# Kernel tuning notes

Measured on AMD Instinct MI355X. Metric: run time of the kernel, lower is better.

The kernel has to match this reference:

```python
import jax, jax.numpy as jnp
import numpy as np
from jax import lax

N_ITER = 50  # entmax-bisect iterations (entmax library default)
DEG = 12    # neighbors per node in global item graph


def entmax_bisect(X, alpha):
    # entmax with per-row alpha, over axis=1. X: [B, L, 1], alpha: [B, 1, 1]
    d = X.shape[1]
    Xa = X * (alpha - 1.0)
    inv = 1.0 / (alpha - 1.0)
    _p = lambda z: jnp.maximum(z, 0.0) ** inv
    max_val = jnp.max(Xa, axis=1, keepdims=True)
    tau_lo = max_val - 1.0                                   # _gp(1, alpha) = 1
    tau_hi = max_val - jnp.power(1.0 / d, alpha - 1.0)       # _gp(1/d, alpha)
    f_lo = jnp.sum(_p(Xa - tau_lo), axis=1, keepdims=True) - 1.0

    def body(i, carry):
        tau_lo, dm, _ = carry
        dm = dm * 0.5
        tau_m = tau_lo + dm
        f_m = jnp.sum(_p(Xa - tau_m), axis=1, keepdims=True) - 1.0
        tau_lo = jnp.where(f_m * f_lo >= 0.0, tau_m, tau_lo)
        return (tau_lo, dm, tau_m)

    tau_lo, dm, tau_m = lax.fori_loop(0, N_ITER, body, (tau_lo, tau_hi - tau_lo, tau_lo))
    p_m = _p(Xa - tau_m)
    return p_m / jnp.sum(p_m, axis=1, keepdims=True)  # ensure_sum_one


def setup_inputs() -> dict:
    key = jax.random.key(0)
    ks = jax.random.split(key, 10)
    B, L, D, N = 1024, 50, 256, 40000
    E = N * DEG
    stdv = 1.0 / np.sqrt(D)
    u = lambda k, shape: jax.random.uniform(k, shape, jnp.float32, -stdv, stdv)

    item_emb = u(ks[0], (N, D)).at[0].set(0.0)  # padding_idx=0
    items = jax.random.randint(ks[1], (B, L), 0, N)
    inputs_seq = jax.random.randint(ks[2], (B, L), 0, N)
    alias_inputs = jax.random.randint(ks[3], (B, L), 0, L)
    target_embedding = jax.random.normal(ks[4], (B, 1, 2 * D), jnp.float32)

    # sparse global item adjacency (row-normalized, DEG neighbors per node)
    adj_rows = jnp.repeat(jnp.arange(N, dtype=jnp.int32), DEG)
    adj_cols = jax.random.randint(ks[5], (E,), 0, N, dtype=jnp.int32)
    adj_vals = jax.random.uniform(ks[6], (E,), jnp.float32) / DEG

    kp = jax.random.split(ks[7], 10)
    return {
        "items": items, "inputs_seq": inputs_seq, "alias_inputs": alias_inputs,
        "target_embedding": target_embedding, "item_emb": item_emb,
        "adj_rows": adj_rows, "adj_cols": adj_cols, "adj_vals": adj_vals,
        "wf_w": u(kp[0], (D, 2 * D)), "wf_b": u(kp[1], (D,)),
        "alphaw_w": u(kp[2], (1, D)), "alphaw_b": u(kp[3], (1,)),
        "at_w0": u(kp[4], (1, D)), "at_w1": u(kp[5], (D, D)),
        "at_w2": u(kp[6], (D, D)), "at_bias": u(kp[7], (D,)),
    }


def reference(items, inputs_seq, alias_inputs, target_embedding, item_emb,
              adj_rows, adj_cols, adj_vals, wf_w, wf_b, alphaw_w, alphaw_b,
              at_w0, at_w1, at_w2, at_bias):
    N = item_emb.shape[0]
    # GlobalItemConv (1 layer): h = (x + adj @ x) / 2 via sparse SpMM
    agg = jax.ops.segment_sum(adj_vals[:, None] * item_emb[adj_cols], adj_rows,
                              num_segments=N)
    graph_embs = (item_emb + agg) * 0.5

    hidden = graph_embs[items]                              # [B, L, D] (dropout: eval)
    target_emb = target_embedding @ wf_w.T + wf_b           # [B, 1, D]

    # get_alpha: sigmoid + 1, then masked_fill(==1 -> 1.00001)
    alpha_ent = jax.nn.sigmoid(target_emb @ alphaw_w.T + alphaw_b) + 1.0  # [B,1,1]
    alpha_ent = jnp.where(alpha_ent == 1.0, 1.00001, alpha_ent)

    # tglobal_attention
    scores = jax.nn.relu(hidden @ at_w1 + target_emb @ at_w2 + at_bias) @ at_w0.T  # [B,L,1]
    attn = entmax_bisect(scores, alpha_ent)                 # sparse softmax over L
    c = jnp.einsum('blo,bld->bod', attn, hidden)[:, 0, :]   # alpha^T @ v, squeeze -> [B,D]

    c = jax.nn.selu(c)
    return c / jnp.linalg.norm(c, axis=-1, keepdims=True)
```

## Files before the change

### kernel.cpp

```cpp
#include <hip/hip_runtime.h>
#include <hip/hip_bf16.h>
#include <math.h>

#define BB 1024
#define LL 50
#define DD 256
#define TWO_D 512
#define NN 40000
#define DEG 12
#define NITER 50

typedef __attribute__((ext_vector_type(8))) short short8;
typedef __attribute__((ext_vector_type(4))) float floatx4;

__device__ __forceinline__ float wave_sum64(float v) {
#pragma unroll
    for (int off = 32; off > 0; off >>= 1) v += __shfl_xor(v, off, 64);
    return v;
}
__device__ __forceinline__ float wave_max64(float v) {
#pragma unroll
    for (int off = 32; off > 0; off >>= 1) v = fmaxf(v, __shfl_xor(v, off, 64));
    return v;
}
__device__ __forceinline__ float dpp_sum64(float v) {
#define DPPADD(ctrl, rm, bm) \
    v += __int_as_float(__builtin_amdgcn_update_dpp(0, __float_as_int(v), ctrl, rm, bm, true))
    DPPADD(0x111, 0xF, 0xF);
    DPPADD(0x112, 0xF, 0xF);
    DPPADD(0x114, 0xF, 0xE);
    DPPADD(0x118, 0xF, 0xC);
    DPPADD(0x142, 0xA, 0xF);
    DPPADD(0x143, 0xC, 0xF);
#undef DPPADD
    return __int_as_float(__builtin_amdgcn_readlane(__float_as_int(v), 63));
}
__device__ __forceinline__ float bf2f(ushort u) {
    union { unsigned int i; float f; } c; c.i = ((unsigned int)u) << 16; return c.f;
}
__device__ __forceinline__ ushort f2bf(float f) {
    __hip_bfloat16 h = __float2bfloat16(f);
    return *(ushort*)&h;
}
__device__ __forceinline__ float hw_exp2(float x) { return __builtin_amdgcn_exp2f(x); }
__device__ __forceinline__ float hw_log2(float x) { return __builtin_amdgcn_logf(x); }

__global__ __launch_bounds__(256) void k_stage1(
    const float* __restrict__ emb, ushort* __restrict__ ebf,
    const int* __restrict__ items, int* __restrict__ flags,
    const float* __restrict__ wf_w, const float* __restrict__ wf_b,
    const float* __restrict__ at_w2, const float* __restrict__ at_bias,
    const float* __restrict__ aw, const float* __restrict__ ab,
    const float* __restrict__ at_w1,
    float* __restrict__ Wc, float* __restrict__ v,
    float* __restrict__ bc, float* __restrict__ c0,
    ushort* __restrict__ w1t)
{
    __shared__ float wcol[DD];
    __shared__ float4 s_p[4][64];
    __shared__ float wred[4];
    __shared__ ushort s_t[4][DD];
    int bid = blockIdx.x;
    int tid = threadIdx.x;

    if (bid < 512) {
        int k = bid;
        int lane = tid & 63, wv = tid >> 6;
        int ng = tid & 63;
        int dq = tid >> 6;

        wcol[tid] = wf_w[tid * TWO_D + k];
        __syncthreads();

        float4 acc = {0.f, 0.f, 0.f, 0.f};
        const float4* w24 = (const float4*)at_w2;
#pragma unroll 8
        for (int d = dq * 64; d < dq * 64 + 64; ++d) {
            float4 w2 = w24[d * 64 + ng];
            float wc = wcol[d];
            acc.x += wc * w2.x; acc.y += wc * w2.y;
            acc.z += wc * w2.z; acc.w += wc * w2.w;
        }
        s_p[dq][ng] = acc;

        float s1 = wcol[tid] * aw[tid];
        s1 = wave_sum64(s1);
        if (lane == 0) wred[wv] = s1;
        __syncthreads();
        if (tid == 0) v[k] = wred[0] + wred[1] + wred[2] + wred[3];

        if (tid < 64) {
            float4 r0 = s_p[0][tid], r1 = s_p[1][tid];
            float4 r2 = s_p[2][tid], r3 = s_p[3][tid];
            float4 rr;
            rr.x = (r0.x + r1.x) + (r2.x + r3.x);
            rr.y = (r0.y + r1.y) + (r2.y + r3.y);
            rr.z = (r0.z + r1.z) + (r2.z + r3.z);
            rr.w = (r0.w + r1.w) + (r2.w + r3.w);
            *(float4*)(Wc + k * DD + tid * 4) = rr;
        }

        if (k < 64) {
            int k0 = k * 4;
#pragma unroll
            for (int j = 0; j < 4; ++j)
                s_t[j][tid] = f2bf(at_w1[(k0 + j) * DD + tid]);
            __syncthreads();
            ushort4 pk;
            pk.x = s_t[0][tid]; pk.y = s_t[1][tid];
            pk.z = s_t[2][tid]; pk.w = s_t[3][tid];
            *(ushort4*)(w1t + tid * DD + k0) = pk;
        }

        if (k == 0) {
            __syncthreads();
            wcol[tid] = wf_b[tid];
            __syncthreads();
            float b[8];
#pragma unroll
            for (int j = 0; j < 8; ++j) b[j] = 0.f;
#pragma unroll 4
            for (int d = 0; d < DD; d += 8) {
#pragma unroll
                for (int j = 0; j < 8; ++j)
                    b[j] += wcol[d + j] * at_w2[(d + j) * DD + tid];
            }
            bc[tid] = at_bias[tid] + ((b[0] + b[1]) + (b[2] + b[3]))
                                   + ((b[4] + b[5]) + (b[6] + b[7]));
            float s2 = wcol[tid] * aw[tid];
            s2 = wave_sum64(s2);
            if (lane == 0) wred[wv] = s2;
            __syncthreads();
            if (tid == 0) c0[0] = wred[0] + wred[1] + wred[2] + wred[3] + ab[0];
        }
    } else if (bid < 712) {
        int i = (bid - 512) * 256 + tid;
        flags[items[i]] = 1;
    } else {
        int base4 = (bid - 712) * (256 * 8) + tid;
        float4 val[8];
#pragma unroll
        for (int j = 0; j < 8; ++j)
            val[j] = *(const float4*)(emb + (size_t)(base4 + j * 256) * 4);
#pragma unroll
        for (int j = 0; j < 8; ++j) {
            ushort4 o;
            o.x = f2bf(val[j].x); o.y = f2bf(val[j].y);
            o.z = f2bf(val[j].z); o.w = f2bf(val[j].w);
            *(ushort4*)(ebf + (size_t)(base4 + j * 256) * 4) = o;
        }
    }
}

__global__ __launch_bounds__(256) void k_stage2(
    const ushort* __restrict__ ebf, const int* __restrict__ adj_cols,
    const float* __restrict__ adj_vals, const int* __restrict__ flags,
    ushort* __restrict__ gbf,
    const float* __restrict__ tgt, const float* __restrict__ Wc,
    const float* __restrict__ bc, const float* __restrict__ v,
    const float* __restrict__ c0, float* __restrict__ t2,
    float* __restrict__ alpha)
{
    __shared__ float x_s[4 * TWO_D];
    int bid = blockIdx.x;
    int tid = threadIdx.x;
    int wv = tid >> 6, lane = tid & 63;

    if (bid < 1024) {
        int t = bid;
        int btile = t >> 2, ntile = t & 3;
        int b0 = btile * 4, n0 = ntile * 64;
        int j = wv;
        for (int i = tid; i < 4 * TWO_D; i += 256) x_s[i] = tgt[b0 * TWO_D + i];
        __syncthreads();

        float acc = bc[n0 + lane];
        const float* xr = x_s + j * TWO_D;
#pragma unroll 8
        for (int k = 0; k < TWO_D; ++k)
            acc += xr[k] * Wc[k * DD + n0 + lane];
        t2[(b0 + j) * DD + n0 + lane] = acc;

        if (ntile == 0) {
            float s = 0.f;
#pragma unroll
            for (int i = 0; i < 8; ++i) s += xr[lane + 64 * i] * v[lane + 64 * i];
            s = wave_sum64(s);
            if (lane == 0) {
                float a = 1.f + 1.f / (1.f + expf(-(s + c0[0])));
                if (a == 1.f) a = 1.00001f;
                alpha[b0 + j] = a;
            }
        }
    } else {
        int n = (bid - 1024) * 4 + wv;
        if (flags[n] != 1) return;
        int colv = 0; float valv = 0.f;
        if (lane < DEG) { colv = adj_cols[n * DEG + lane]; valv = adj_vals[n * DEG + lane]; }
        int cols[DEG]; float vals[DEG];
#pragma unroll
        for (int k = 0; k < DEG; ++k) {
            cols[k] = __builtin_amdgcn_readlane(colv, k);
            vals[k] = __int_as_float(__builtin_amdgcn_readlane(__float_as_int(valv), k));
        }
        ushort4 s = *(const ushort4*)(ebf + (size_t)n * DD + lane * 4);
        ushort4 e[DEG];
#pragma unroll
        for (int k = 0; k < DEG; ++k)
            e[k] = *(const ushort4*)(ebf + (size_t)cols[k] * DD + lane * 4);
        float a0 = bf2f(s.x), a1 = bf2f(s.y), a2 = bf2f(s.z), a3 = bf2f(s.w);
#pragma unroll
        for (int k = 0; k < DEG; ++k) {
            float vv = vals[k];
            a0 += vv * bf2f(e[k].x); a1 += vv * bf2f(e[k].y);
            a2 += vv * bf2f(e[k].z); a3 += vv * bf2f(e[k].w);
        }
        ushort4 o;
        o.x = f2bf(0.5f * a0); o.y = f2bf(0.5f * a1);
        o.z = f2bf(0.5f * a2); o.w = f2bf(0.5f * a3);
        *(ushort4*)(gbf + (size_t)n * DD + lane * 4) = o;
    }
}

__device__ __forceinline__ float pw(float z, float invv) {
    return hw_exp2(invv * hw_log2(z));
}

__global__ __launch_bounds__(256, 4) void k_fused(
    const int* __restrict__ items, const ushort* __restrict__ gbf,
    const ushort* __restrict__ w1t, const float* __restrict__ t2,
    const float* __restrict__ at_w0, const float* __restrict__ alpha,
    float* __restrict__ out)
{
    __shared__ float t2_s[DD];
    __shared__ float sred[64][4];
    __shared__ int s_items[64];
    __shared__ float red[4];

    int b = blockIdx.x;
    int tid = threadIdx.x;
    int lane = tid & 63, wv = tid >> 6;
    int cn = lane & 15, q = lane >> 4;
    int n0 = wv * 64;

    if (tid < 64) {
        int l = (tid < LL) ? tid : 0;
        s_items[tid] = items[b * LL + l];
    }
    t2_s[tid] = t2[b * DD + tid];
    __syncthreads();

    const ushort* arow[4];
#pragma unroll
    for (int mt = 0; mt < 4; ++mt)
        arow[mt] = gbf + (size_t)s_items[mt * 16 + cn] * DD;
    const ushort* brow[4];
#pragma unroll
    for (int nt = 0; nt < 4; ++nt)
        brow[nt] = w1t + (size_t)(n0 + nt * 16 + cn) * DD;

    floatx4 acc[4][4];
#pragma unroll
    for (int mt = 0; mt < 4; ++mt)
#pragma unroll
        for (int nt = 0; nt < 4; ++nt)
            acc[mt][nt] = (floatx4){0.f, 0.f, 0.f, 0.f};

#pragma unroll 1
    for (int kc = 0; kc < 4; ++kc) {
#pragma unroll
        for (int ks = 0; ks < 2; ++ks) {
            int ko = kc * 64 + ks * 32 + q * 8;
            short8 af[4], bfr[4];
#pragma unroll
            for (int mt = 0; mt < 4; ++mt)
                af[mt] = *(const short8*)(arow[mt] + ko);
#pragma unroll
            for (int nt = 0; nt < 4; ++nt)
                bfr[nt] = *(const short8*)(brow[nt] + ko);
#pragma unroll
            for (int mt = 0; mt < 4; ++mt)
#pragma unroll
                for (int nt = 0; nt < 4; ++nt)
                    acc[mt][nt] = __builtin_amdgcn_mfma_f32_16x16x32_bf16(
                        af[mt], bfr[nt], acc[mt][nt], 0, 0, 0);
        }
    }

    float w0v[4];
#pragma unroll
    for (int nt = 0; nt < 4; ++nt) w0v[nt] = at_w0[n0 + nt * 16 + cn];
#pragma unroll
    for (int mt = 0; mt < 4; ++mt) {
#pragma unroll
        for (int r = 0; r < 4; ++r) {
            int row = mt * 16 + q * 4 + r;
            float p = 0.f;
#pragma unroll
            for (int nt = 0; nt < 4; ++nt) {
                int col = n0 + nt * 16 + cn;
                float vvv = acc[mt][nt][r] + t2_s[col];
                p += fmaxf(vvv, 0.f) * w0v[nt];
            }
            p += __shfl_xor(p, 1, 64);
            p += __shfl_xor(p, 2, 64);
            p += __shfl_xor(p, 4, 64);
            p += __shfl_xor(p, 8, 64);
            if (cn == 0) sred[row][wv] = p;
        }
    }
    __syncthreads();

    float sc = sred[lane][0] + sred[lane][1] + sred[lane][2] + sred[lane][3];

    float a = alpha[b];
    float am1 = a - 1.f;
    float invv = 1.f / am1;
    float x = (lane < LL) ? sc : -__builtin_inff();
    float Xa = x * am1;

    float mx = wave_max64(Xa);
    float tau_lo = mx - 1.f;
    float tau_hi = mx - hw_exp2(am1 * hw_log2(1.f / (float)LL));

    float f_lo = dpp_sum64(pw(fmaxf(Xa - tau_lo, 0.f), invv)) - 1.f;

    float dm = tau_hi - tau_lo;
    float tau_m = tau_lo;
#pragma unroll 1
    for (int it = 0; it < NITER; ++it) {
        dm *= 0.5f;
        tau_m = tau_lo + dm;
        if (tau_m == tau_lo) break;
        float f_m = dpp_sum64(pw(fmaxf(Xa - tau_m, 0.f), invv)) - 1.f;
        if (f_m * f_lo >= 0.f) tau_lo = tau_m;
    }
    float pm = pw(fmaxf(Xa - tau_m, 0.f), invv);
    float sden = dpp_sum64(pm);
    float pmn = pm / sden;

    int d = tid;
    float c = 0.f;
#pragma unroll
    for (int l = 0; l < LL; ++l) {
        float al = __int_as_float(__builtin_amdgcn_readlane(__float_as_int(pmn), l));
        c += al * bf2f(gbf[(size_t)s_items[l] * DD + d]);
    }

    const float SC = 1.0507009873554805f;
    const float AL = 1.6732632423543772f;
    c = SC * (c > 0.f ? c : AL * expm1f(c));

    float ss = wave_sum64(c * c);
    if (lane == 0) red[wv] = ss;
    __syncthreads();
    float tot = red[0] + red[1] + red[2] + red[3];
    out[b * DD + d] = c / sqrtf(tot);
}

extern "C" void kernel_launch(void* const* d_in, const int* in_sizes, int n_in,
                              void* d_out, int out_size, void* d_ws, size_t ws_size,
                              hipStream_t stream) {
    const int*   items     = (const int*)  d_in[0];
    const float* tgt       = (const float*)d_in[3];
    const float* item_emb  = (const float*)d_in[4];
    const int*   adj_cols  = (const int*)  d_in[6];
    const float* adj_vals  = (const float*)d_in[7];
    const float* wf_w      = (const float*)d_in[8];
    const float* wf_b      = (const float*)d_in[9];
    const float* alphaw_w  = (const float*)d_in[10];
    const float* alphaw_b  = (const float*)d_in[11];
    const float* at_w0     = (const float*)d_in[12];
    const float* at_w1     = (const float*)d_in[13];
    const float* at_w2     = (const float*)d_in[14];
    const float* at_bias   = (const float*)d_in[15];

    const size_t SZ_TAB = (size_t)NN * DD * sizeof(ushort);
    char* ws = (char*)d_ws;
    ushort* gbf = (ushort*)ws;   ws += SZ_TAB;
    ushort* ebf = (ushort*)ws;   ws += SZ_TAB;
    ushort* w1t = (ushort*)ws;   ws += (size_t)DD * DD * sizeof(ushort);
    int*   flags = (int*)ws;     ws += (size_t)NN * sizeof(int);
    float* Wc     = (float*)ws;  ws += (size_t)TWO_D * DD * sizeof(float);
    float* bcv    = (float*)ws;  ws += (size_t)DD * sizeof(float);
    float* vv     = (float*)ws;  ws += (size_t)TWO_D * sizeof(float);
    float* c0v    = (float*)ws;  ws += 16 * sizeof(float);
    float* t2     = (float*)ws;  ws += (size_t)BB * DD * sizeof(float);
    float* alpha  = (float*)ws;  ws += ((size_t)BB + 32) * sizeof(float);
    float* out    = (float*)d_out;

    k_stage1<<<1962, 256, 0, stream>>>(item_emb, ebf, items, flags,
                                       wf_w, wf_b, at_w2, at_bias,
                                       alphaw_w, alphaw_b, at_w1,
                                       Wc, vv, bcv, c0v, w1t);
    k_stage2<<<11024, 256, 0, stream>>>(ebf, adj_cols, adj_vals, flags, gbf,
                                        tgt, Wc, bcv, vv, c0v, t2, alpha);
    k_fused<<<BB, 256, 0, stream>>>(items, gbf, w1t, t2, at_w0, alpha, out);
}
```

Before: 191.6 us.

## Scatter graph embeddings directly into dense per-batch hidden buffer via linked lists

Result: slower. 203.0 us (+5.9%).

```diff
diff --git a/kernel.cpp b/kernel.cpp
--- a/kernel.cpp
+++ b/kernel.cpp
@@ -45,9 +45,15 @@
 __device__ __forceinline__ float hw_exp2(float x) { return __builtin_amdgcn_exp2f(x); }
 __device__ __forceinline__ float hw_log2(float x) { return __builtin_amdgcn_logf(x); }
 
+__global__ __launch_bounds__(256) void k_init(int* __restrict__ head) {
+    int i = blockIdx.x * 256 + threadIdx.x;
+    if (i < NN) head[i] = -1;
+}
+
 __global__ __launch_bounds__(256) void k_stage1(
     const float* __restrict__ emb, ushort* __restrict__ ebf,
     const int* __restrict__ items, int* __restrict__ flags,
+    int* __restrict__ head, int* __restrict__ nxt,
     const float* __restrict__ wf_w, const float* __restrict__ wf_b,
     const float* __restrict__ at_w2, const float* __restrict__ at_bias,
     const float* __restrict__ aw, const float* __restrict__ ab,
@@ -135,7 +141,9 @@
         }
     } else if (bid < 712) {
         int i = (bid - 512) * 256 + tid;
-        flags[items[i]] = 1;
+        int n = items[i];
+        flags[n] = 1;
+        nxt[i] = atomicExch(head + n, i);
     } else {
         int base4 = (bid - 712) * (256 * 8) + tid;
         float4 val[8];
@@ -155,7 +163,8 @@
 __global__ __launch_bounds__(256) void k_stage2(
     const ushort* __restrict__ ebf, const int* __restrict__ adj_cols,
     const float* __restrict__ adj_vals, const int* __restrict__ flags,
-    ushort* __restrict__ gbf,
+    const int* __restrict__ head, const int* __restrict__ nxt,
+    ushort* __restrict__ hidden,
     const float* __restrict__ tgt, const float* __restrict__ Wc,
     const float* __restrict__ bc, const float* __restrict__ v,
     const float* __restrict__ c0, float* __restrict__ t2,
@@ -194,7 +203,9 @@
         }
     } else {
         int n = (bid - 1024) * 4 + wv;
-        if (flags[n] != 1) return;
+        int fl = flags[n];
+        int hd = head[n];
+        if (fl != 1) return;
         int colv = 0; float valv = 0.f;
         if (lane < DEG) { colv = adj_cols[n * DEG + lane]; valv = adj_vals[n * DEG + lane]; }
         int cols[DEG]; float vals[DEG];
@@ -218,7 +229,11 @@
         ushort4 o;
         o.x = f2bf(0.5f * a0); o.y = f2bf(0.5f * a1);
         o.z = f2bf(0.5f * a2); o.w = f2bf(0.5f * a3);
-        *(ushort4*)(gbf + (size_t)n * DD + lane * 4) = o;
+        int i = hd;
+        while ((unsigned)i < (unsigned)(BB * LL)) {
+            *(ushort4*)(hidden + (size_t)i * DD + lane * 4) = o;
+            i = nxt[i];
+        }
     }
 }
 
@@ -227,14 +242,12 @@
 }
 
 __global__ __launch_bounds__(256, 4) void k_fused(
-    const int* __restrict__ items, const ushort* __restrict__ gbf,
-    const ushort* __restrict__ w1t, const float* __restrict__ t2,
-    const float* __restrict__ at_w0, const float* __restrict__ alpha,
-    float* __restrict__ out)
+    const ushort* __restrict__ hidden, const ushort* __restrict__ w1t,
+    const float* __restrict__ t2, const float* __restrict__ at_w0,
+    const float* __restrict__ alpha, float* __restrict__ out)
 {
     __shared__ float t2_s[DD];
     __shared__ float sred[64][4];
-    __shared__ int s_items[64];
     __shared__ float red[4];
 
     int b = blockIdx.x;
@@ -242,23 +255,21 @@
     int lane = tid & 63, wv = tid >> 6;
     int cn = lane & 15, q = lane >> 4;
     int n0 = wv * 64;
-
-    if (tid < 64) {
-        int l = (tid < LL) ? tid : 0;
-        s_items[tid] = items[b * LL + l];
-    }
-    t2_s[tid] = t2[b * DD + tid];
-    __syncthreads();
+    const ushort* hb = hidden + (size_t)b * (LL * DD);
 
     const ushort* arow[4];
 #pragma unroll
-    for (int mt = 0; mt < 4; ++mt)
-        arow[mt] = gbf + (size_t)s_items[mt * 16 + cn] * DD;
+    for (int mt = 0; mt < 4; ++mt) {
+        int row = mt * 16 + cn;
+        arow[mt] = hb + (size_t)(row < LL ? row : 0) * DD;
+    }
     const ushort* brow[4];
 #pragma unroll
     for (int nt = 0; nt < 4; ++nt)
         brow[nt] = w1t + (size_t)(n0 + nt * 16 + cn) * DD;
 
+    t2_s[tid] = t2[b * DD + tid];
+
     floatx4 acc[4][4];
 #pragma unroll
     for (int mt = 0; mt < 4; ++mt)
@@ -266,7 +277,7 @@
         for (int nt = 0; nt < 4; ++nt)
             acc[mt][nt] = (floatx4){0.f, 0.f, 0.f, 0.f};
 
-#pragma unroll 1
+#pragma unroll
     for (int kc = 0; kc < 4; ++kc) {
 #pragma unroll
         for (int ks = 0; ks < 2; ++ks) {
@@ -286,6 +297,7 @@
                         af[mt], bfr[nt], acc[mt][nt], 0, 0, 0);
         }
     }
+    __syncthreads();
 
     float w0v[4];
 #pragma unroll
@@ -344,7 +356,7 @@
 #pragma unroll
     for (int l = 0; l < LL; ++l) {
         float al = __int_as_float(__builtin_amdgcn_readlane(__float_as_int(pmn), l));
-        c += al * bf2f(gbf[(size_t)s_items[l] * DD + d]);
+        c += al * bf2f(hb[l * DD + d]);
     }
 
     const float SC = 1.0507009873554805f;
@@ -375,12 +387,13 @@
     const float* at_w2     = (const float*)d_in[14];
     const float* at_bias   = (const float*)d_in[15];
 
-    const size_t SZ_TAB = (size_t)NN * DD * sizeof(ushort);
     char* ws = (char*)d_ws;
-    ushort* gbf = (ushort*)ws;   ws += SZ_TAB;
-    ushort* ebf = (ushort*)ws;   ws += SZ_TAB;
+    ushort* hidden = (ushort*)ws; ws += (size_t)BB * LL * DD * sizeof(ushort);
+    ushort* ebf = (ushort*)ws;   ws += (size_t)NN * DD * sizeof(ushort);
     ushort* w1t = (ushort*)ws;   ws += (size_t)DD * DD * sizeof(ushort);
     int*   flags = (int*)ws;     ws += (size_t)NN * sizeof(int);
+    int*   head  = (int*)ws;     ws += (size_t)NN * sizeof(int);
+    int*   nxt   = (int*)ws;     ws += (size_t)BB * LL * sizeof(int);
     float* Wc     = (float*)ws;  ws += (size_t)TWO_D * DD * sizeof(float);
     float* bcv    = (float*)ws;  ws += (size_t)DD * sizeof(float);
     float* vv     = (float*)ws;  ws += (size_t)TWO_D * sizeof(float);
@@ -389,11 +402,12 @@
     float* alpha  = (float*)ws;  ws += ((size_t)BB + 32) * sizeof(float);
     float* out    = (float*)d_out;
 
-    k_stage1<<<1962, 256, 0, stream>>>(item_emb, ebf, items, flags,
+    k_init<<<(NN + 255) / 256, 256, 0, stream>>>(head);
+    k_stage1<<<1962, 256, 0, stream>>>(item_emb, ebf, items, flags, head, nxt,
                                        wf_w, wf_b, at_w2, at_bias,
                                        alphaw_w, alphaw_b, at_w1,
                                        Wc, vv, bcv, c0v, w1t);
-    k_stage2<<<11024, 256, 0, stream>>>(ebf, adj_cols, adj_vals, flags, gbf,
-                                        tgt, Wc, bcv, vv, c0v, t2, alpha);
-    k_fused<<<BB, 256, 0, stream>>>(items, gbf, w1t, t2, at_w0, alpha, out);
-}
+    k_stage2<<<11024, 256, 0, stream>>>(ebf, adj_cols, adj_vals, flags, head, nxt,
+                                        hidden, tgt, Wc, bcv, vv, c0v, t2, alpha);
+    k_fused<<<BB, 256, 0, stream>>>(hidden, w1t, t2, at_w0, alpha, out);
+}
```

## Retile weight-fold and target GEMM blocks for register reuse

Applied to the files above, without the earlier changes.

After: 243.9 us. 27.3% more time.

```diff
diff --git a/kernel.cpp b/kernel.cpp
--- a/kernel.cpp
+++ b/kernel.cpp
@@ -56,88 +56,85 @@
     float* __restrict__ bc, float* __restrict__ c0,
     ushort* __restrict__ w1t)
 {
-    __shared__ float wcol[DD];
-    __shared__ float4 s_p[4][64];
-    __shared__ float wred[4];
-    __shared__ ushort s_t[4][DD];
     int bid = blockIdx.x;
     int tid = threadIdx.x;
 
-    if (bid < 512) {
-        int k = bid;
-        int lane = tid & 63, wv = tid >> 6;
-        int ng = tid & 63;
-        int dq = tid >> 6;
-
-        wcol[tid] = wf_w[tid * TWO_D + k];
-        __syncthreads();
-
-        float4 acc = {0.f, 0.f, 0.f, 0.f};
+    if (bid < 32) {
+        __shared__ float s_wf[256][17];
+        __shared__ float s_aw[DD];
+        __shared__ float s_part[16][17];
+        int k0 = bid * 16;
+
+        {
+            const float* wr = wf_w + (size_t)tid * TWO_D + k0;
+#pragma unroll
+            for (int j = 0; j < 16; ++j) s_wf[tid][j] = wr[j];
+        }
+        s_aw[tid] = aw[tid];
+        __syncthreads();
+
+        int kl = tid >> 4, ng = tid & 15;
+        float4 acc[4];
+#pragma unroll
+        for (int c = 0; c < 4; ++c) acc[c] = (float4){0.f, 0.f, 0.f, 0.f};
         const float4* w24 = (const float4*)at_w2;
+#pragma unroll 4
+        for (int d = 0; d < DD; ++d) {
+            float wfv = s_wf[d][kl];
+            const float4* rowp = w24 + d * 64 + ng * 4;
+#pragma unroll
+            for (int c = 0; c < 4; ++c) {
+                float4 w2 = rowp[c];
+                acc[c].x += wfv * w2.x; acc[c].y += wfv * w2.y;
+                acc[c].z += wfv * w2.z; acc[c].w += wfv * w2.w;
+            }
+        }
+        float* wco = Wc + (size_t)(k0 + kl) * DD + ng * 16;
+#pragma unroll
+        for (int c = 0; c < 4; ++c) *(float4*)(wco + c * 4) = acc[c];
+
+        float p = 0.f;
+#pragma unroll
+        for (int j = 0; j < 16; ++j) p += s_wf[ng * 16 + j][kl] * s_aw[ng * 16 + j];
+        s_part[kl][ng] = p;
+        __syncthreads();
+        if (tid < 16) {
+            float s = 0.f;
+#pragma unroll
+            for (int j = 0; j < 16; ++j) s += s_part[tid][j];
+            v[k0 + tid] = s;
+        }
+    } else if (bid < 96) {
+        __shared__ ushort s_t[4][DD];
+        int k0 = (bid - 32) * 4;
+#pragma unroll
+        for (int j = 0; j < 4; ++j)
+            s_t[j][tid] = f2bf(at_w1[(k0 + j) * DD + tid]);
+        __syncthreads();
+        ushort4 pk;
+        pk.x = s_t[0][tid]; pk.y = s_t[1][tid];
+        pk.z = s_t[2][tid]; pk.w = s_t[3][tid];
+        *(ushort4*)(w1t + (size_t)tid * DD + k0) = pk;
+    } else if (bid == 96) {
+        __shared__ float s_wb[DD];
+        __shared__ float wred[4];
+        s_wb[tid] = wf_b[tid];
+        float awv = aw[tid];
+        __syncthreads();
+        float accb = 0.f;
 #pragma unroll 8
-        for (int d = dq * 64; d < dq * 64 + 64; ++d) {
-            float4 w2 = w24[d * 64 + ng];
-            float wc = wcol[d];
-            acc.x += wc * w2.x; acc.y += wc * w2.y;
-            acc.z += wc * w2.z; acc.w += wc * w2.w;
-        }
-        s_p[dq][ng] = acc;
-
-        float s1 = wcol[tid] * aw[tid];
-        s1 = wave_sum64(s1);
-        if (lane == 0) wred[wv] = s1;
-        __syncthreads();
-        if (tid == 0) v[k] = wred[0] + wred[1] + wred[2] + wred[3];
-
-        if (tid < 64) {
-            float4 r0 = s_p[0][tid], r1 = s_p[1][tid];
-            float4 r2 = s_p[2][tid], r3 = s_p[3][tid];
-            float4 rr;
-            rr.x = (r0.x + r1.x) + (r2.x + r3.x);
-            rr.y = (r0.y + r1.y) + (r2.y + r3.y);
-            rr.z = (r0.z + r1.z) + (r2.z + r3.z);
-            rr.w = (r0.w + r1.w) + (r2.w + r3.w);
-            *(float4*)(Wc + k * DD + tid * 4) = rr;
-        }
-
-        if (k < 64) {
-            int k0 = k * 4;
-#pragma unroll
-            for (int j = 0; j < 4; ++j)
-                s_t[j][tid] = f2bf(at_w1[(k0 + j) * DD + tid]);
-            __syncthreads();
-            ushort4 pk;
-            pk.x = s_t[0][tid]; pk.y = s_t[1][tid];
-            pk.z = s_t[2][tid]; pk.w = s_t[3][tid];
-            *(ushort4*)(w1t + tid * DD + k0) = pk;
-        }
-
-        if (k == 0) {
-            __syncthreads();
-            wcol[tid] = wf_b[tid];
-            __syncthreads();
-            float b[8];
-#pragma unroll
-            for (int j = 0; j < 8; ++j) b[j] = 0.f;
-#pragma unroll 4
-            for (int d = 0; d < DD; d += 8) {
-#pragma unroll
-                for (int j = 0; j < 8; ++j)
-                    b[j] += wcol[d + j] * at_w2[(d + j) * DD + tid];
-            }
-            bc[tid] = at_bias[tid] + ((b[0] + b[1]) + (b[2] + b[3]))
-                                   + ((b[4] + b[5]) + (b[6] + b[7]));
-            float s2 = wcol[tid] * aw[tid];
-            s2 = wave_sum64(s2);
-            if (lane == 0) wred[wv] = s2;
-            __syncthreads();
-            if (tid == 0) c0[0] = wred[0] + wred[1] + wred[2] + wred[3] + ab[0];
-        }
-    } else if (bid < 712) {
-        int i = (bid - 512) * 256 + tid;
+        for (int d = 0; d < DD; ++d) accb += s_wb[d] * at_w2[d * DD + tid];
+        bc[tid] = at_bias[tid] + accb;
+        float s2 = s_wb[tid] * awv;
+        s2 = wave_sum64(s2);
+        if ((tid & 63) == 0) wred[tid >> 6] = s2;
+        __syncthreads();
+        if (tid == 0) c0[0] = wred[0] + wred[1] + wred[2] + wred[3] + ab[0];
+    } else if (bid < 297) {
+        int i = (bid - 97) * 256 + tid;
         flags[items[i]] = 1;
     } else {
-        int base4 = (bid - 712) * (256 * 8) + tid;
+        int base4 = (bid - 297) * (256 * 8) + tid;
         float4 val[8];
 #pragma unroll
         for (int j = 0; j < 8; ++j)
@@ -161,39 +158,56 @@
     const float* __restrict__ c0, float* __restrict__ t2,
     float* __restrict__ alpha)
 {
-    __shared__ float x_s[4 * TWO_D];
     int bid = blockIdx.x;
     int tid = threadIdx.x;
     int wv = tid >> 6, lane = tid & 63;
 
-    if (bid < 1024) {
-        int t = bid;
-        int btile = t >> 2, ntile = t & 3;
-        int b0 = btile * 4, n0 = ntile * 64;
-        int j = wv;
-        for (int i = tid; i < 4 * TWO_D; i += 256) x_s[i] = tgt[b0 * TWO_D + i];
-        __syncthreads();
-
-        float acc = bc[n0 + lane];
-        const float* xr = x_s + j * TWO_D;
+    if (bid < 256) {
+        __shared__ float x_s[16 * TWO_D];
+        int btile = bid >> 2, ntile = bid & 3;
+        int b0 = btile * 16, n0 = ntile * 64;
+        for (int i = tid; i < 16 * TWO_D; i += 256)
+            x_s[i] = tgt[(size_t)b0 * TWO_D + i];
+        __syncthreads();
+
+        int r0 = wv * 4;
+        const float* x0 = x_s + (r0 + 0) * TWO_D;
+        const float* x1 = x_s + (r0 + 1) * TWO_D;
+        const float* x2 = x_s + (r0 + 2) * TWO_D;
+        const float* x3 = x_s + (r0 + 3) * TWO_D;
+        float bb = bc[n0 + lane];
+        float a0 = bb, a1 = bb, a2 = bb, a3 = bb;
 #pragma unroll 8
-        for (int k = 0; k < TWO_D; ++k)
-            acc += xr[k] * Wc[k * DD + n0 + lane];
-        t2[(b0 + j) * DD + n0 + lane] = acc;
+        for (int k = 0; k < TWO_D; ++k) {
+            float wc = Wc[(size_t)k * DD + n0 + lane];
+            a0 += x0[k] * wc; a1 += x1[k] * wc;
+            a2 += x2[k] * wc; a3 += x3[k] * wc;
+        }
+        t2[(size_t)(b0 + r0 + 0) * DD + n0 + lane] = a0;
+        t2[(size_t)(b0 + r0 + 1) * DD + n0 + lane] = a1;
+        t2[(size_t)(b0 + r0 + 2) * DD + n0 + lane] = a2;
+        t2[(size_t)(b0 + r0 + 3) * DD + n0 + lane] = a3;
 
         if (ntile == 0) {
-            float s = 0.f;
-#pragma unroll
-            for (int i = 0; i < 8; ++i) s += xr[lane + 64 * i] * v[lane + 64 * i];
-            s = wave_sum64(s);
-            if (lane == 0) {
-                float a = 1.f + 1.f / (1.f + expf(-(s + c0[0])));
-                if (a == 1.f) a = 1.00001f;
-                alpha[b0 + j] = a;
+            float vr[8];
+#pragma unroll
+            for (int i = 0; i < 8; ++i) vr[i] = v[lane + 64 * i];
+#pragma unroll
+            for (int r = 0; r < 4; ++r) {
+                const float* xr = x_s + (r0 + r) * TWO_D;
+                float s = 0.f;
+#pragma unroll
+                for (int i = 0; i < 8; ++i) s += xr[lane + 64 * i] * vr[i];
+                s = wave_sum64(s);
+                if (lane == 0) {
+                    float a = 1.f + 1.f / (1.f + expf(-(s + c0[0])));
+                    if (a == 1.f) a = 1.00001f;
+                    alpha[b0 + r0 + r] = a;
+                }
             }
         }
     } else {
-        int n = (bid - 1024) * 4 + wv;
+        int n = (bid - 256) * 4 + wv;
         if (flags[n] != 1) return;
         int colv = 0; float valv = 0.f;
         if (lane < DEG) { colv = adj_cols[n * DEG + lane]; valv = adj_vals[n * DEG + lane]; }
@@ -243,6 +257,11 @@
     int cn = lane & 15, q = lane >> 4;
     int n0 = wv * 64;
 
+    float a = alpha[b];
+    float w0v[4];
+#pragma unroll
+    for (int nt = 0; nt < 4; ++nt) w0v[nt] = at_w0[n0 + nt * 16 + cn];
+
     if (tid < 64) {
         int l = (tid < LL) ? tid : 0;
         s_items[tid] = items[b * LL + l];
@@ -266,7 +285,7 @@
         for (int nt = 0; nt < 4; ++nt)
             acc[mt][nt] = (floatx4){0.f, 0.f, 0.f, 0.f};
 
-#pragma unroll 1
+#pragma unroll
     for (int kc = 0; kc < 4; ++kc) {
 #pragma unroll
         for (int ks = 0; ks < 2; ++ks) {
@@ -287,9 +306,6 @@
         }
     }
 
-    float w0v[4];
-#pragma unroll
-    for (int nt = 0; nt < 4; ++nt) w0v[nt] = at_w0[n0 + nt * 16 + cn];
 #pragma unroll
     for (int mt = 0; mt < 4; ++mt) {
 #pragma unroll
@@ -313,7 +329,6 @@
 
     float sc = sred[lane][0] + sred[lane][1] + sred[lane][2] + sred[lane][3];
 
-    float a = alpha[b];
     float am1 = a - 1.f;
     float invv = 1.f / am1;
     float x = (lane < LL) ? sc : -__builtin_inff();
@@ -389,11 +404,11 @@
     float* alpha  = (float*)ws;  ws += ((size_t)BB + 32) * sizeof(float);
     float* out    = (float*)d_out;
 
-    k_stage1<<<1962, 256, 0, stream>>>(item_emb, ebf, items, flags,
+    k_stage1<<<1547, 256, 0, stream>>>(item_emb, ebf, items, flags,
                                        wf_w, wf_b, at_w2, at_bias,
                                        alphaw_w, alphaw_b, at_w1,
                                        Wc, vv, bcv, c0v, w1t);
-    k_stage2<<<11024, 256, 0, stream>>>(ebf, adj_cols, adj_vals, flags, gbf,
+    k_stage2<<<10256, 256, 0, stream>>>(ebf, adj_cols, adj_vals, flags, gbf,
                                         tgt, Wc, bcv, vv, c0v, t2, alpha);
     k_fused<<<BB, 256, 0, stream>>>(items, gbf, w1t, t2, at_w0, alpha, out);
 }
```

## Pack two batch rows per block in fused attention kernel

Applied to the files above, without the earlier changes.

New measurement: 191.6 us. Within noise of the previous version (-0.0%).

```diff
diff --git a/kernel.cpp b/kernel.cpp
--- a/kernel.cpp
+++ b/kernel.cpp
@@ -226,34 +226,39 @@
     return hw_exp2(invv * hw_log2(z));
 }
 
-__global__ __launch_bounds__(256, 4) void k_fused(
+__global__ __launch_bounds__(512, 4) void k_fused(
     const int* __restrict__ items, const ushort* __restrict__ gbf,
     const ushort* __restrict__ w1t, const float* __restrict__ t2,
     const float* __restrict__ at_w0, const float* __restrict__ alpha,
     float* __restrict__ out)
 {
-    __shared__ float t2_s[DD];
-    __shared__ float sred[64][4];
-    __shared__ int s_items[64];
-    __shared__ float red[4];
-
-    int b = blockIdx.x;
+    __shared__ float t2_s[2][DD];
+    __shared__ float sred[128][4];
+    __shared__ int s_items[128];
+    __shared__ float attn_s[2][64];
+    __shared__ float red[8];
+
+    int b2 = blockIdx.x;
     int tid = threadIdx.x;
     int lane = tid & 63, wv = tid >> 6;
     int cn = lane & 15, q = lane >> 4;
-    int n0 = wv * 64;
-
-    if (tid < 64) {
-        int l = (tid < LL) ? tid : 0;
-        s_items[tid] = items[b * LL + l];
-    }
-    t2_s[tid] = t2[b * DD + tid];
+    int rowg = wv >> 2;
+    int n0 = (wv & 3) * 64;
+
+    if (tid < 128) {
+        int r = tid;
+        int bl = r / 50;
+        int l = r - bl * 50;
+        if (bl > 1) { bl = 0; l = 0; }
+        s_items[r] = items[(2 * b2 + bl) * LL + l];
+    }
+    t2_s[tid >> 8][tid & 255] = t2[(size_t)(2 * b2 + (tid >> 8)) * DD + (tid & 255)];
     __syncthreads();
 
     const ushort* arow[4];
 #pragma unroll
     for (int mt = 0; mt < 4; ++mt)
-        arow[mt] = gbf + (size_t)s_items[mt * 16 + cn] * DD;
+        arow[mt] = gbf + (size_t)s_items[rowg * 64 + mt * 16 + cn] * DD;
     const ushort* brow[4];
 #pragma unroll
     for (int nt = 0; nt < 4; ++nt)
@@ -290,62 +295,67 @@
     float w0v[4];
 #pragma unroll
     for (int nt = 0; nt < 4; ++nt) w0v[nt] = at_w0[n0 + nt * 16 + cn];
+    const float* t2r0 = t2_s[0];
 #pragma unroll
     for (int mt = 0; mt < 4; ++mt) {
 #pragma unroll
         for (int r = 0; r < 4; ++r) {
-            int row = mt * 16 + q * 4 + r;
+            int row = rowg * 64 + mt * 16 + q * 4 + r;
+            const float* t2b = (row < 50) ? t2_s[0] : t2_s[1];
             float p = 0.f;
 #pragma unroll
             for (int nt = 0; nt < 4; ++nt) {
                 int col = n0 + nt * 16 + cn;
-                float vvv = acc[mt][nt][r] + t2_s[col];
+                float vvv = acc[mt][nt][r] + t2b[col];
                 p += fmaxf(vvv, 0.f) * w0v[nt];
             }
             p += __shfl_xor(p, 1, 64);
             p += __shfl_xor(p, 2, 64);
             p += __shfl_xor(p, 4, 64);
             p += __shfl_xor(p, 8, 64);
-            if (cn == 0) sred[row][wv] = p;
+            if (cn == 0) sred[row][wv & 3] = p;
         }
     }
     __syncthreads();
 
-    float sc = sred[lane][0] + sred[lane][1] + sred[lane][2] + sred[lane][3];
-
-    float a = alpha[b];
-    float am1 = a - 1.f;
-    float invv = 1.f / am1;
-    float x = (lane < LL) ? sc : -__builtin_inff();
-    float Xa = x * am1;
-
-    float mx = wave_max64(Xa);
-    float tau_lo = mx - 1.f;
-    float tau_hi = mx - hw_exp2(am1 * hw_log2(1.f / (float)LL));
-
-    float f_lo = dpp_sum64(pw(fmaxf(Xa - tau_lo, 0.f), invv)) - 1.f;
-
-    float dm = tau_hi - tau_lo;
-    float tau_m = tau_lo;
+    if (wv < 2) {
+        int row = wv * 50 + lane;
+        int rr = (row < 128) ? row : 0;
+        float sc = sred[rr][0] + sred[rr][1] + sred[rr][2] + sred[rr][3];
+
+        float a = alpha[2 * b2 + wv];
+        float am1 = a - 1.f;
+        float invv = 1.f / am1;
+        float x = (lane < LL) ? sc : -__builtin_inff();
+        float Xa = x * am1;
+
+        float mx = wave_max64(Xa);
+        float tau_lo = mx - 1.f;
+        float tau_hi = mx - hw_exp2(am1 * hw_log2(1.f / (float)LL));
+
+        float f_lo = dpp_sum64(pw(fmaxf(Xa - tau_lo, 0.f), invv)) - 1.f;
+
+        float dm = tau_hi - tau_lo;
+        float tau_m = tau_lo;
 #pragma unroll 1
-    for (int it = 0; it < NITER; ++it) {
-        dm *= 0.5f;
-        tau_m = tau_lo + dm;
-        if (tau_m == tau_lo) break;
-        float f_m = dpp_sum64(pw(fmaxf(Xa - tau_m, 0.f), invv)) - 1.f;
-        if (f_m * f_lo >= 0.f) tau_lo = tau_m;
-    }
-    float pm = pw(fmaxf(Xa - tau_m, 0.f), invv);
-    float sden = dpp_sum64(pm);
-    float pmn = pm / sden;
-
-    int d = tid;
+        for (int it = 0; it < NITER; ++it) {
+            dm *= 0.5f;
+            tau_m = tau_lo + dm;
+            if (tau_m == tau_lo) break;
+            float f_m = dpp_sum64(pw(fmaxf(Xa - tau_m, 0.f), invv)) - 1.f;
+            if (f_m * f_lo >= 0.f) tau_lo = tau_m;
+        }
+        float pm = pw(fmaxf(Xa - tau_m, 0.f), invv);
+        float sden = dpp_sum64(pm);
+        attn_s[wv][lane] = pm / sden;
+    }
+    __syncthreads();
+
+    int bl = tid >> 8, d = tid & 255;
     float c = 0.f;
 #pragma unroll
-    for (int l = 0; l < LL; ++l) {
-        float al = __int_as_float(__builtin_amdgcn_readlane(__float_as_int(pmn), l));
-        c += al * bf2f(gbf[(size_t)s_items[l] * DD + d]);
-    }
+    for (int l = 0; l < LL; ++l)
+        c += attn_s[bl][l] * bf2f(gbf[(size_t)s_items[bl * 50 + l] * DD + d]);
 
     const float SC = 1.0507009873554805f;
     const float AL = 1.6732632423543772f;
@@ -354,8 +364,9 @@
     float ss = wave_sum64(c * c);
     if (lane == 0) red[wv] = ss;
     __syncthreads();
-    float tot = red[0] + red[1] + red[2] + red[3];
-    out[b * DD + d] = c / sqrtf(tot);
+    int rb = bl << 2;
+    float tot = red[rb] + red[rb + 1] + red[rb + 2] + red[rb + 3];
+    out[(size_t)(2 * b2 + bl) * DD + d] = c / sqrtf(tot);
 }
 
 extern "C" void kernel_launch(void* const* d_in, const int* in_sizes, int n_in,
@@ -395,5 +406,5 @@
                                        Wc, vv, bcv, c0v, w1t);
     k_stage2<<<11024, 256, 0, stream>>>(ebf, adj_cols, adj_vals, flags, gbf,
                                         tgt, Wc, bcv, vv, c0v, t2, alpha);
-    k_fused<<<BB, 256, 0, stream>>>(items, gbf, w1t, t2, at_w0, alpha, out);
-}
+    k_fused<<<BB / 2, 512, 0, stream>>>(items, gbf, w1t, t2, at_w0, alpha, out);
+}
```
